# Optimization experiments

Measured on AMD Instinct MI355X. Metric: run time of the kernel, lower is better.

The kernel has to match this reference:

```python
import math
import jax, jax.numpy as jnp
import numpy as np

B, T = 16, 576
HG = WG = 24          # grid_size
DIN = DOUT = 768
NH, HD = 12, 64       # n_heads, head_dim
LD = 256              # latent_dim
SCALES = (1, 2, 4)


def _rel_idx(s):
    """Replicates _build_rel_pos_indices for scale s (static numpy constants)."""
    gh, gw = HG // s, WG // s
    qh, qw = np.meshgrid(np.arange(HG), np.arange(WG), indexing='ij')
    qh, qw = qh.reshape(-1), qw.reshape(-1)                      # (T,)
    kh = np.arange(gh) * s + (s - 1) / 2.0                       # pooled key centers
    kw = np.arange(gw) * s + (s - 1) / 2.0
    kh2, kw2 = np.meshgrid(kh, kw, indexing='ij')
    kh2, kw2 = kh2.reshape(-1), kw2.reshape(-1)                  # (gh*gw,)
    # .astype(int64) truncates toward zero, matching torch .long()
    rel_h = (qh[:, None] - kh2[None, :]).astype(np.int64) + (HG - 1)
    rel_w = (qw[:, None] - kw2[None, :]).astype(np.int64) + (gw - 1)
    return jnp.asarray(rel_h * (2 * gw - 1) + rel_w)             # (T, gh*gw)


def setup_inputs() -> dict:
    key = jax.random.key(0)
    ks = jax.random.split(key, 16)
    std = 0.02
    inp = {
        'x': jax.random.normal(ks[0], (B, T, DIN), dtype=jnp.float32),
        'wq': jax.random.normal(ks[1], (DIN, DOUT), dtype=jnp.float32) * std,
        'wdkv': jax.random.normal(ks[2], (DIN, LD), dtype=jnp.float32) * std,
        'wuk1': jax.random.normal(ks[3], (LD, DOUT), dtype=jnp.float32) * std,
        'wuk2': jax.random.normal(ks[4], (LD, DOUT), dtype=jnp.float32) * std,
        'wuk4': jax.random.normal(ks[5], (LD, DOUT), dtype=jnp.float32) * std,
        'wuv1': jax.random.normal(ks[6], (LD, DOUT), dtype=jnp.float32) * std,
        'wuv2': jax.random.normal(ks[7], (LD, DOUT), dtype=jnp.float32) * std,
        'wuv4': jax.random.normal(ks[8], (LD, DOUT), dtype=jnp.float32) * std,
        'wout': jax.random.normal(ks[12], (DOUT, DOUT), dtype=jnp.float32) * std,
        'bout': jnp.zeros((DOUT,), dtype=jnp.float32),
    }
    # rel-pos bias tables: table_h = 2*HG-1 = 47; table_w = 2*(WG//s)-1
    for j, s in enumerate(SCALES):
        tw = 2 * (WG // s) - 1
        inp[f'tbl{s}'] = jax.random.normal(ks[9 + j], (NH, (2 * HG - 1) * tw),
                                           dtype=jnp.float32) * std
    return inp


def reference(x, wq, wdkv, wuk1, wuk2, wuk4, wuv1, wuv2, wuv4,
              tbl1, tbl2, tbl4, wout, bout):
    b = x.shape[0]
    q = (x @ wq).reshape(b, T, NH, HD).transpose(0, 2, 1, 3)     # (B,H,T,hd)
    lat = x @ wdkv                                                # (B,T,LD)
    lat_sp = lat.reshape(b, HG, WG, LD)
    wuks, wuvs = (wuk1, wuk2, wuk4), (wuv1, wuv2, wuv4)
    tbls = (tbl1, tbl2, tbl4)
    scale = 1.0 / math.sqrt(HD)
    out = jnp.zeros((b, NH, T, HD), x.dtype)
    for i, s in enumerate(SCALES):
        gh, gw = HG // s, WG // s
        if s > 1:  # exact s x s mean pooling (adaptive pool with divisible dims)
            lp = lat_sp.reshape(b, gh, s, gw, s, LD).mean(axis=(2, 4))
        else:
            lp = lat_sp
        lseq = lp.reshape(b, gh * gw, LD)
        k = (lseq @ wuks[i]).reshape(b, gh * gw, NH, HD).transpose(0, 2, 1, 3)
        v = (lseq @ wuvs[i]).reshape(b, gh * gw, NH, HD).transpose(0, 2, 1, 3)
        bias = tbls[i][:, _rel_idx(s)]                            # (H,T,K) gather
        scores = jnp.einsum('bhqd,bhkd->bhqk', q, k) * scale + bias[None]
        w = jax.nn.softmax(scores, axis=-1)
        out = out + jnp.einsum('bhqk,bhkd->bhqd', w, v)
    out = out / len(SCALES)
    ctx = out.transpose(0, 2, 1, 3).reshape(b, T, DOUT)
    return ctx @ wout + bout
```

## Files before the change

kernel.cpp:

```cpp
#include <hip/hip_runtime.h>
#include <hip/hip_bf16.h>
#include <math.h>

#define B_   16
#define T_   576
#define NH_  12

typedef unsigned short u16;
typedef __attribute__((ext_vector_type(8))) short bf16x8;
typedef __attribute__((ext_vector_type(4))) float f32x4;

__device__ __forceinline__ float bf2f(u16 u) {
    union { unsigned int i; float f; } x; x.i = ((unsigned int)u) << 16; return x.f;
}
__device__ __forceinline__ u16 f2bf(float f) {
    union { float f; unsigned int i; } x; x.f = f;
    unsigned int r = x.i + 0x7fffu + ((x.i >> 16) & 1u);
    return (u16)(r >> 16);
}
__device__ __forceinline__ void splitf(float v, u16& h, u16& l) {
    h = f2bf(v);
    l = f2bf(v - bf2f(h));
}
__device__ __forceinline__ void gld_lds16(const u16* g, u16* l) {
    __builtin_amdgcn_global_load_lds(
        (const __attribute__((address_space(1))) unsigned int*)g,
        (__attribute__((address_space(3))) unsigned int*)l, 16, 0, 0);
}
__device__ __forceinline__ float exp2f_(float x) {
#if __has_builtin(__builtin_amdgcn_exp2f)
    return __builtin_amdgcn_exp2f(x);
#else
    return exp2f(x);
#endif
}

__global__ __launch_bounds__(256)
void convert_bf(const float* __restrict__ in, u16* __restrict__ out, int n) {
    const int i8 = (blockIdx.x * 256 + threadIdx.x) * 8;
    if (i8 >= n) return;
    const float4 a = *(const float4*)&in[i8];
    const float4 b = *(const float4*)&in[i8 + 4];
    u16 o[8] = {f2bf(a.x),f2bf(a.y),f2bf(a.z),f2bf(a.w),
                f2bf(b.x),f2bf(b.y),f2bf(b.z),f2bf(b.w)};
    *(bf16x8*)&out[i8] = *(bf16x8*)o;
}

__global__ __launch_bounds__(256)
void prep_weights(const float* __restrict__ wq, const float* __restrict__ wdkv,
                  const float* __restrict__ uk1, const float* __restrict__ uv1,
                  const float* __restrict__ uk2, const float* __restrict__ uv2,
                  const float* __restrict__ uk4, const float* __restrict__ uv4,
                  const float* __restrict__ wout,
                  u16* wqT, u16* wdkvT, u16* uk1T, u16* uv1T, u16* uk2T,
                  u16* uv2T, u16* uk4T, u16* uv4T, u16* woutTh, u16* woutTl) {
    int id = blockIdx.x;
    const float* W; u16* Th; u16* Tl = nullptr; int K, N, gx; bool split = false;
    if (id < 576)       { W = wq;  Th = wqT;  K = 768; N = 768; gx = 24; }
    else if (id < 768)  { id -= 576; W = wdkv; Th = wdkvT; K = 768; N = 256; gx = 8; }
    else if (id < 1920) {
        id -= 768; const int w = id / 192; id -= w * 192;
        const float* Ws[6] = {uk1, uv1, uk2, uv2, uk4, uv4};
        u16* Ts[6] = {uk1T, uv1T, uk2T, uv2T, uk4T, uv4T};
        W = Ws[w]; Th = Ts[w]; K = 256; N = 768; gx = 24;
    } else { id -= 1920; W = wout; Th = woutTh; Tl = woutTl; K = 768; N = 768; gx = 24; split = true; }
    const int bx = id % gx, by = id / gx;
    const int n0 = bx * 32, k0 = by * 32;

    __shared__ float t[32][33];
    const int tid = threadIdx.x;
    const int c  = tid & 31;
    const int r4 = tid >> 5;
#pragma unroll
    for (int i = 0; i < 4; ++i)
        t[r4*4+i][c] = W[(size_t)(k0 + r4*4 + i) * N + n0 + c];
    __syncthreads();
#pragma unroll
    for (int i = 0; i < 4; ++i) {
        const float v = t[c][r4*4+i];
        const size_t o = (size_t)(n0 + r4*4 + i) * K + k0 + c;
        if (split) { u16 h, l; splitf(v, h, l); Th[o] = h; Tl[o] = l; }
        else       { Th[o] = f2bf(v); }
    }
}

template<bool IN_SPLIT, int OM1, int OM2, bool HAS_BIAS>
__global__ __launch_bounds__(256, 2)
void gemm_mfma(const u16* __restrict__ Ah, const u16* __restrict__ Al,
               const u16* __restrict__ B1h, const u16* __restrict__ B1l,
               const u16* __restrict__ B2h,
               const float* __restrict__ bias, float* __restrict__ C1f,
               u16* __restrict__ C1bf, u16* __restrict__ C2bf,
               int M, int N1, int N2, int K, int KSt) {
    __shared__ u16 smem[(IN_SPLIT ? 4 : 2) * 8192];
    const int tid  = threadIdx.x;
    const int wid  = tid >> 6;
    const int lane = tid & 63;
    const int lr   = lane & 15;
    const int kg   = lane >> 4;
    const int wr   = wid >> 1, wc = wid & 1;
    const int m0   = blockIdx.y * 128;
    const int n0   = blockIdx.x * 128;
    const bool second = (OM2 >= 0) && (n0 >= N1);
    const int nb   = second ? n0 - N1 : n0;
    const int subrow = lane >> 3;
    const int gslot  = (lane & 7) ^ subrow;

    const u16* src; int rowbase; bool isA; u16* tile;
    constexpr int NITER = IN_SPLIT ? 16 : 8;
    if (IN_SPLIT) {
        src = (wid == 0) ? Ah : (wid == 1) ? Al : (wid == 2) ? B1h : B1l;
        rowbase = (wid < 2) ? m0 : n0;
        isA = (wid < 2);
        tile = smem + wid * 8192;
    } else {
        const u16* Bsel = second ? B2h : B1h;
        src = (wid < 2) ? Ah : Bsel;
        rowbase = ((wid < 2) ? m0 : nb) + (wid & 1) * 64;
        isA = (wid < 2);
        tile = smem + (wid >> 1) * 8192 + (wid & 1) * 4096;
    }

    f32x4 acc[4][4];
#pragma unroll
    for (int i = 0; i < 4; ++i)
#pragma unroll
        for (int j = 0; j < 4; ++j) acc[i][j] = (f32x4)(0.f);

    for (int k0 = 0; k0 < K; k0 += 64) {
#pragma unroll
        for (int i = 0; i < NITER; ++i) {
            int grow = rowbase + i*8 + subrow;
            if (isA && grow >= M) grow = M - 1;
            gld_lds16(src + (size_t)grow * K + (k0 + gslot * 8), tile + i * 512);
        }
        __syncthreads();
#pragma unroll
        for (int ks = 0; ks < 2; ++ks) {
            const int slot = (ks*4 + kg) ^ (lr & 7);
            bf16x8 ah[4], bh[4], al[4], bl[4];
#pragma unroll
            for (int i = 0; i < 4; ++i) {
                const int offA = (wr*64 + i*16 + lr) * 64 + slot * 8;
                const int offB = (wc*64 + i*16 + lr) * 64 + slot * 8;
                ah[i] = *(const bf16x8*)(smem + offA);
                bh[i] = *(const bf16x8*)(smem + (IN_SPLIT ? 16384 : 8192) + offB);
                if (IN_SPLIT) {
                    al[i] = *(const bf16x8*)(smem + 8192  + offA);
                    bl[i] = *(const bf16x8*)(smem + 24576 + offB);
                }
            }
#pragma unroll
            for (int i = 0; i < 4; ++i)
#pragma unroll
                for (int j = 0; j < 4; ++j) {
                    acc[i][j] = __builtin_amdgcn_mfma_f32_16x16x32_bf16(ah[i], bh[j], acc[i][j], 0, 0, 0);
                    if (IN_SPLIT) {
                        acc[i][j] = __builtin_amdgcn_mfma_f32_16x16x32_bf16(ah[i], bl[j], acc[i][j], 0, 0, 0);
                        acc[i][j] = __builtin_amdgcn_mfma_f32_16x16x32_bf16(al[i], bh[j], acc[i][j], 0, 0, 0);
                    }
                }
        }
        __syncthreads();
    }
    const int rb = lane >> 4;
    float bv[4];
    if (HAS_BIAS) {
#pragma unroll
        for (int j = 0; j < 4; ++j) bv[j] = bias[n0 + wc*64 + j*16 + lr];
    }
#pragma unroll
    for (int i = 0; i < 4; ++i)
#pragma unroll
        for (int e = 0; e < 4; ++e) {
            const int row = m0 + wr*64 + i*16 + rb*4 + e;
            if (row < M) {
#pragma unroll
                for (int j = 0; j < 4; ++j) {
                    const int colw = wc*64 + j*16 + lr;
                    float v = acc[i][j][e];
                    if (HAS_BIAS) v += bv[j];
                    if (!second) {
                        const int col = n0 + colw;
                        if (OM1 == 0) C1f[(size_t)row * N1 + col] = v;
                        else if (OM1 == 1) C1bf[(size_t)row * N1 + col] = f2bf(v);
                        else {
                            const int bidx = row / KSt, key = row - bidx * KSt;
                            C1bf[((size_t)bidx * N1 + col) * KSt + key] = f2bf(v);
                        }
                    } else {
                        const int col = nb + colw;
                        if (OM2 == 1) C2bf[(size_t)row * N2 + col] = f2bf(v);
                        else if (OM2 == 2) {
                            const int bidx = row / KSt, key = row - bidx * KSt;
                            C2bf[((size_t)bidx * N2 + col) * KSt + key] = f2bf(v);
                        }
                    }
                }
            }
        }
}

__global__ __launch_bounds__(256)
void pool_both(const u16* __restrict__ lat, u16* __restrict__ lp2,
               u16* __restrict__ lp4) {
    const int c = threadIdx.x;
    int id = blockIdx.x;
    if (id < 2304) {
        const int b = id / 144, g = id - b*144;
        const int gh = g / 12, gw = g - gh*12;
        const size_t i0 = (((size_t)(b*24 + gh*2))*24 + gw*2)*256 + c;
        const float s = (bf2f(lat[i0]) + bf2f(lat[i0+256]) +
                         bf2f(lat[i0+24*256]) + bf2f(lat[i0+24*256+256])) * 0.25f;
        lp2[(size_t)id*256 + c] = f2bf(s);
    } else {
        id -= 2304;
        const int b = id / 36, g = id - b*36;
        const int gh = g / 6, gw = g - gh*6;
        const size_t base = (((size_t)(b*24 + gh*4))*24 + gw*4)*256 + c;
        float s = 0.f;
#pragma unroll
        for (int i = 0; i < 4; ++i)
#pragma unroll
            for (int j = 0; j < 4; ++j)
                s += bf2f(lat[base + (size_t)(i*24 + j)*256]);
        lp4[(size_t)id*256 + c] = f2bf(s * (1.f/16.f));
    }
}

template<int KS, int GW, int S>
__device__ __forceinline__ void attn_scale(
    const u16* __restrict__ Kbf, const u16* __restrict__ Vt,
    const float* __restrict__ TBL,
    const bf16x8 qa[2], int qh, int qw, int b, int h,
    int tid, int lr, int kg,
    u16 (*Kl)[72], u16 (*Vl)[72], u16* PlW, float* TblL,
    f32x4 octx[4])
{
    constexpr int TW  = 2*GW - 1;
    constexpr int NT  = (KS + 63) / 64;
    constexpr int NTB = 47 * TW;
    constexpr float C1 = 0.18033688011112042f;

    __syncthreads();
    for (int i = tid; i < NTB; i += 256)
        TblL[i] = TBL[(size_t)h * NTB + i] * 1.4426950408889634f;

    const int base1 = (qh + 23)*TW + qw + (GW - 1);
    f32x4 pacc[4];
#pragma unroll
    for (int j = 0; j < 4; ++j) pacc[j] = (f32x4)(0.f);
    float ls = 0.f;

    const int keyS = tid & 63;
    const int c2   = tid >> 6;

    for (int t = 0; t < NT; ++t) {
        const int kt0 = t * 64;
        __syncthreads();
        {
            const u16* kp = Kbf + ((size_t)b*KS + kt0 + keyS)*768 + h*64;
            *(bf16x8*)&Kl[keyS][c2*8]     = *(const bf16x8*)(kp + c2*8);
            *(bf16x8*)&Kl[keyS][(c2+4)*8] = *(const bf16x8*)(kp + (c2+4)*8);
            const u16* vp = Vt + ((size_t)b*768 + h*64 + keyS)*KS;
            const int kb0 = kt0 + c2*8;
            const int kb1 = kt0 + 32 + c2*8;
            if ((KS % 8) == 0 && ((KS % 64) == 0 || kb0 + 8 <= KS)) {
                *(bf16x8*)&Vl[keyS][c2*8] = *(const bf16x8*)(vp + kb0);
            } else {
                bf16x8 vv = {0,0,0,0,0,0,0,0};
#pragma unroll
                for (int u = 0; u < 8; ++u) if (kb0 + u < KS) vv[u] = (short)vp[kb0+u];
                *(bf16x8*)&Vl[keyS][c2*8] = vv;
            }
            if ((KS % 8) == 0 && ((KS % 64) == 0 || kb1 + 8 <= KS)) {
                *(bf16x8*)&Vl[keyS][(c2+4)*8] = *(const bf16x8*)(vp + kb1);
            } else {
                bf16x8 vv = {0,0,0,0,0,0,0,0};
#pragma unroll
                for (int u = 0; u < 8; ++u) if (kb1 + u < KS) vv[u] = (short)vp[kb1+u];
                *(bf16x8*)&Vl[keyS][(c2+4)*8] = vv;
            }
        }
        __syncthreads();

        f32x4 sf[4] = {(f32x4)(0.f), (f32x4)(0.f), (f32x4)(0.f), (f32x4)(0.f)};
        __builtin_amdgcn_s_setprio(1);
#pragma unroll
        for (int ks = 0; ks < 2; ++ks)
#pragma unroll
            for (int g = 0; g < 4; ++g) {
                const bf16x8 kb = *(const bf16x8*)&Kl[g*16 + lr][ks*32 + kg*8];
                sf[g] = __builtin_amdgcn_mfma_f32_16x16x32_bf16(kb, qa[ks], sf[g], 0, 0, 0);
            }
        __builtin_amdgcn_s_setprio(0);

#pragma unroll
        for (int g = 0; g < 4; ++g) {
            const int key0 = kt0 + g*16 + kg*4;
            const bool v4 = ((KS % 64) == 0) || (key0 < KS);
            const int khi  = key0 / GW;
            const int kwi0 = key0 - khi*GW;
            float pv[4];
            if (S == 1) {
                const int idx0 = base1 - khi*TW - kwi0;
#pragma unroll
                for (int e = 0; e < 4; ++e)
                    pv[e] = exp2f_(fmaf(sf[g][e], C1, TblL[idx0 - e]));
            } else if (S == 2) {
                const int dh = qh - 2*khi;
                const int rh = dh - (dh >= 1) + 23;
#pragma unroll
                for (int e = 0; e < 4; ++e) {
                    const int dw = qw - 2*(kwi0 + e);
                    const int rw = dw - (dw >= 1) + (GW - 1);
                    const float x = fmaf(sf[g][e], C1, TblL[rh*TW + rw]);
                    pv[e] = v4 ? exp2f_(x) : 0.f;
                }
            } else {
#pragma unroll
                for (int e = 0; e < 4; ++e) {
                    int kk = kwi0 + e;
                    const int wrap = (kk >= GW);
                    kk -= wrap ? GW : 0;
                    const int kh2 = khi + wrap;
                    const int dh = qh - 4*kh2;
                    const int dw = qw - 4*kk;
                    const int rh = dh - 1 - (dh >= 2) + 23;
                    const int rw = dw - 1 - (dw >= 2) + (GW - 1);
                    const float x = fmaf(sf[g][e], C1, TblL[rh*TW + rw]);
                    pv[e] = v4 ? exp2f_(x) : 0.f;
                }
            }
            ls += (pv[0] + pv[1]) + (pv[2] + pv[3]);
            const unsigned int plo = (unsigned int)f2bf(pv[0]) | ((unsigned int)f2bf(pv[1]) << 16);
            const unsigned int phi = (unsigned int)f2bf(pv[2]) | ((unsigned int)f2bf(pv[3]) << 16);
            *(uint2*)&PlW[lr*72 + g*16 + kg*4] = make_uint2(plo, phi);
        }

        __builtin_amdgcn_s_setprio(1);
#pragma unroll
        for (int ks = 0; ks < 2; ++ks) {
            const bf16x8 pb = *(const bf16x8*)&PlW[lr*72 + ks*32 + kg*8];
#pragma unroll
            for (int j = 0; j < 4; ++j) {
                const bf16x8 vb = *(const bf16x8*)&Vl[j*16 + lr][ks*32 + kg*8];
                pacc[j] = __builtin_amdgcn_mfma_f32_16x16x32_bf16(vb, pb, pacc[j], 0, 0, 0);
            }
        }
        __builtin_amdgcn_s_setprio(0);
    }

    ls += __shfl_xor(ls, 16);
    ls += __shfl_xor(ls, 32);
    const float inv = 1.0f / (3.0f * ls);
#pragma unroll
    for (int j = 0; j < 4; ++j)
#pragma unroll
        for (int e = 0; e < 4; ++e)
            octx[j][e] = fmaf(pacc[j][e], inv, octx[j][e]);
}

__global__ __launch_bounds__(256)
void attn_fused(const u16* __restrict__ Qbf,
                const u16* __restrict__ K1, const u16* __restrict__ V1t,
                const u16* __restrict__ K2, const u16* __restrict__ V2t,
                const u16* __restrict__ K4, const u16* __restrict__ V4t,
                const float* __restrict__ T1, const float* __restrict__ T2,
                const float* __restrict__ T4,
                u16* __restrict__ Ch, u16* __restrict__ Cl) {
    __shared__ u16 Kl[64][72];
    __shared__ u16 Vl[64][72];
    __shared__ u16 Pl[4][16][72];
    __shared__ float TblF[2209];
    const int tid  = threadIdx.x;
    const int wid  = tid >> 6;
    const int lane = tid & 63;
    const int lr   = lane & 15;
    const int kg   = lane >> 4;
    const int bid  = blockIdx.x;
    const int qt   = bid / 192;
    const int bh   = bid - qt*192;
    const int b    = bh / 12;
    const int h    = bh - b*12;
    const int qw0  = qt*64 + wid*16;
    const int q    = qw0 + lr;
    const int qh   = q / 24, qw = q - qh*24;

    bf16x8 qa[2];
    {
        const u16* qp = Qbf + ((size_t)(b*T_) + q)*768 + h*64 + kg*8;
        qa[0] = *(const bf16x8*)qp;
        qa[1] = *(const bf16x8*)(qp + 32);
    }
    f32x4 octx[4];
#pragma unroll
    for (int j = 0; j < 4; ++j) octx[j] = (f32x4)(0.f);
    u16* PlW = &Pl[wid][0][0];

    attn_scale<576,24,1>(K1, V1t, T1, qa, qh, qw, b, h, tid, lr, kg, Kl, Vl, PlW, TblF, octx);
    attn_scale<144,12,2>(K2, V2t, T2, qa, qh, qw, b, h, tid, lr, kg, Kl, Vl, PlW, TblF, octx);
    attn_scale< 36, 6,4>(K4, V4t, T4, qa, qh, qw, b, h, tid, lr, kg, Kl, Vl, PlW, TblF, octx);

    const size_t rowoff = ((size_t)(b*T_) + q)*768 + h*64;
#pragma unroll
    for (int j = 0; j < 4; ++j) {
        ushort4 hv, lv;
        u16 h0,h1,h2,h3, l0,l1,l2,l3;
        splitf(octx[j][0], h0, l0); splitf(octx[j][1], h1, l1);
        splitf(octx[j][2], h2, l2); splitf(octx[j][3], h3, l3);
        hv = make_ushort4(h0,h1,h2,h3); lv = make_ushort4(l0,l1,l2,l3);
        *(ushort4*)&Ch[rowoff + j*16 + kg*4] = hv;
        *(ushort4*)&Cl[rowoff + j*16 + kg*4] = lv;
    }
}

extern "C" void kernel_launch(void* const* d_in, const int* in_sizes, int n_in,
                              void* d_out, int out_size, void* d_ws, size_t ws_size,
                              hipStream_t stream) {
    const float* x    = (const float*)d_in[0];
    const float* wq   = (const float*)d_in[1];
    const float* wdkv = (const float*)d_in[2];
    const float* wuk1 = (const float*)d_in[3];
    const float* wuk2 = (const float*)d_in[4];
    const float* wuk4 = (const float*)d_in[5];
    const float* wuv1 = (const float*)d_in[6];
    const float* wuv2 = (const float*)d_in[7];
    const float* wuv4 = (const float*)d_in[8];
    const float* wout = (const float*)d_in[9];
    const float* bout = (const float*)d_in[10];
    const float* tbl1 = (const float*)d_in[11];
    const float* tbl2 = (const float*)d_in[12];
    const float* tbl4 = (const float*)d_in[13];

    u16* p = (u16*)d_ws;
    u16* x_bf   = p;            p += 7077888;
    u16* q_bf   = p;            p += 7077888;
    u16* lat_bf = p;            p += 2359296;
    u16* lp2_bf = p;            p += 589824;
    u16* lp4_bf = p;            p += 147456;
    u16* wqT    = p;            p += 589824;
    u16* wdkvT  = p;            p += 196608;
    u16* uk1T   = p;            p += 196608;
    u16* uv1T   = p;            p += 196608;
    u16* uk2T   = p;            p += 196608;
    u16* uv2T   = p;            p += 196608;
    u16* uk4T   = p;            p += 196608;
    u16* uv4T   = p;            p += 196608;
    u16* woutTh = p;            p += 589824;
    u16* woutTl = p;            p += 589824;
    u16* k1     = p;            p += 7077888;
    u16* v1t    = p;            p += 7077888;
    u16* k2     = p;            p += 1769472;
    u16* v2t    = p;            p += 1769472;
    u16* k4     = p;            p += 442368;
    u16* v4t    = p;            p += 442368;
    u16* ctxh   = p;            p += 7077888;
    u16* ctxl   = p;            p += 7077888;
    float* outp = (float*)d_out;

    convert_bf<<<3456, 256, 0, stream>>>(x, x_bf, 7077888);
    prep_weights<<<2496, 256, 0, stream>>>(wq, wdkv, wuk1, wuv1, wuk2, wuv2,
                                           wuk4, wuv4, wout,
                                           wqT, wdkvT, uk1T, uv1T, uk2T, uv2T,
                                           uk4T, uv4T, woutTh, woutTl);

    gemm_mfma<false,1,1,false><<<dim3(8,72), 256, 0, stream>>>(
        x_bf, nullptr, wqT, nullptr, wdkvT, nullptr, nullptr, q_bf, lat_bf,
        9216, 768, 256, 768, 0);
    pool_both<<<2880, 256, 0, stream>>>(lat_bf, lp2_bf, lp4_bf);

    gemm_mfma<false,1,2,false><<<dim3(12,72), 256, 0, stream>>>(
        lat_bf, nullptr, uk1T, nullptr, uv1T, nullptr, nullptr, k1, v1t,
        9216, 768, 768, 256, 576);
    gemm_mfma<false,1,2,false><<<dim3(12,18), 256, 0, stream>>>(
        lp2_bf, nullptr, uk2T, nullptr, uv2T, nullptr, nullptr, k2, v2t,
        2304, 768, 768, 256, 144);
    gemm_mfma<false,1,2,false><<<dim3(12,5), 256, 0, stream>>>(
        lp4_bf, nullptr, uk4T, nullptr, uv4T, nullptr, nullptr, k4, v4t,
        576, 768, 768, 256, 36);

    attn_fused<<<9*192, 256, 0, stream>>>(q_bf, k1, v1t, k2, v2t, k4, v4t,
                                          tbl1, tbl2, tbl4, ctxh, ctxl);

    gemm_mfma<true,0,-1,true><<<dim3(6,72), 256, 0, stream>>>(
        ctxh, ctxl, woutTh, woutTl, nullptr, bout, outp, nullptr, nullptr,
        9216, 768, 0, 768, 0);
}
```

Measured before the change: 331.0 us.

## Double-buffer K/V tiles with async LDS loads and merge prep and KV launches

The attention kernel now streams K/V tiles through two LDS buffers with global_load_lds and an XOR swizzle, so the next tile is fetched while the current one is computed. All three scales run as one continuous tile pipeline, and all three bias tables are preloaded once. Separately, the input convert and weight prep are merged into one launch, and the three KV projection GEMMs become a single kernel. The V4 stride is padded to 64 so its tile loads stay in bounds. This cuts launch overhead and global-load stalls, at the cost of more LDS per block (which may lower occupancy) and more complex synchronisation.

After: 293.3 us. 1.13x faster.

```diff
diff --git a/kernel.cpp b/kernel.cpp
--- a/kernel.cpp
+++ b/kernel.cpp
@@ -35,26 +35,32 @@
 #endif
 }
 
+#define VMBAR() do { \
+    asm volatile("s_waitcnt vmcnt(0)" ::: "memory"); \
+    __builtin_amdgcn_s_barrier(); \
+    __builtin_amdgcn_sched_barrier(0); } while (0)
+
 __global__ __launch_bounds__(256)
-void convert_bf(const float* __restrict__ in, u16* __restrict__ out, int n) {
-    const int i8 = (blockIdx.x * 256 + threadIdx.x) * 8;
-    if (i8 >= n) return;
-    const float4 a = *(const float4*)&in[i8];
-    const float4 b = *(const float4*)&in[i8 + 4];
-    u16 o[8] = {f2bf(a.x),f2bf(a.y),f2bf(a.z),f2bf(a.w),
-                f2bf(b.x),f2bf(b.y),f2bf(b.z),f2bf(b.w)};
-    *(bf16x8*)&out[i8] = *(bf16x8*)o;
-}
-
-__global__ __launch_bounds__(256)
-void prep_weights(const float* __restrict__ wq, const float* __restrict__ wdkv,
-                  const float* __restrict__ uk1, const float* __restrict__ uv1,
-                  const float* __restrict__ uk2, const float* __restrict__ uv2,
-                  const float* __restrict__ uk4, const float* __restrict__ uv4,
-                  const float* __restrict__ wout,
-                  u16* wqT, u16* wdkvT, u16* uk1T, u16* uv1T, u16* uk2T,
-                  u16* uv2T, u16* uk4T, u16* uv4T, u16* woutTh, u16* woutTl) {
+void prep_all(const float* __restrict__ x, u16* __restrict__ x_bf,
+              const float* __restrict__ wq, const float* __restrict__ wdkv,
+              const float* __restrict__ uk1, const float* __restrict__ uv1,
+              const float* __restrict__ uk2, const float* __restrict__ uv2,
+              const float* __restrict__ uk4, const float* __restrict__ uv4,
+              const float* __restrict__ wout,
+              u16* wqT, u16* wdkvT, u16* uk1T, u16* uv1T, u16* uk2T,
+              u16* uv2T, u16* uk4T, u16* uv4T, u16* woutTh, u16* woutTl) {
+    __shared__ float t[32][33];
     int id = blockIdx.x;
+    if (id < 3456) {
+        const int i8 = (id * 256 + threadIdx.x) * 8;
+        const float4 a = *(const float4*)&x[i8];
+        const float4 b = *(const float4*)&x[i8 + 4];
+        u16 o[8] = {f2bf(a.x),f2bf(a.y),f2bf(a.z),f2bf(a.w),
+                    f2bf(b.x),f2bf(b.y),f2bf(b.z),f2bf(b.w)};
+        *(bf16x8*)&x_bf[i8] = *(bf16x8*)o;
+        return;
+    }
+    id -= 3456;
     const float* W; u16* Th; u16* Tl = nullptr; int K, N, gx; bool split = false;
     if (id < 576)       { W = wq;  Th = wqT;  K = 768; N = 768; gx = 24; }
     else if (id < 768)  { id -= 576; W = wdkv; Th = wdkvT; K = 768; N = 256; gx = 8; }
@@ -66,8 +72,6 @@
     } else { id -= 1920; W = wout; Th = woutTh; Tl = woutTl; K = 768; N = 768; gx = 24; split = true; }
     const int bx = id % gx, by = id / gx;
     const int n0 = bx * 32, k0 = by * 32;
-
-    __shared__ float t[32][33];
     const int tid = threadIdx.x;
     const int c  = tid & 31;
     const int r4 = tid >> 5;
@@ -85,22 +89,22 @@
 }
 
 template<bool IN_SPLIT, int OM1, int OM2, bool HAS_BIAS>
-__global__ __launch_bounds__(256, 2)
-void gemm_mfma(const u16* __restrict__ Ah, const u16* __restrict__ Al,
+__device__ __forceinline__ void gemm_body(
+               u16* smem, int bx, int by,
+               const u16* __restrict__ Ah, const u16* __restrict__ Al,
                const u16* __restrict__ B1h, const u16* __restrict__ B1l,
                const u16* __restrict__ B2h,
                const float* __restrict__ bias, float* __restrict__ C1f,
                u16* __restrict__ C1bf, u16* __restrict__ C2bf,
-               int M, int N1, int N2, int K, int KSt) {
-    __shared__ u16 smem[(IN_SPLIT ? 4 : 2) * 8192];
+               int M, int N1, int N2, int K, int KStL, int KStS) {
     const int tid  = threadIdx.x;
     const int wid  = tid >> 6;
     const int lane = tid & 63;
     const int lr   = lane & 15;
     const int kg   = lane >> 4;
     const int wr   = wid >> 1, wc = wid & 1;
-    const int m0   = blockIdx.y * 128;
-    const int n0   = blockIdx.x * 128;
+    const int m0   = by * 128;
+    const int n0   = bx * 128;
     const bool second = (OM2 >= 0) && (n0 >= N1);
     const int nb   = second ? n0 - N1 : n0;
     const int subrow = lane >> 3;
@@ -185,20 +189,58 @@
                         if (OM1 == 0) C1f[(size_t)row * N1 + col] = v;
                         else if (OM1 == 1) C1bf[(size_t)row * N1 + col] = f2bf(v);
                         else {
-                            const int bidx = row / KSt, key = row - bidx * KSt;
-                            C1bf[((size_t)bidx * N1 + col) * KSt + key] = f2bf(v);
+                            const int bidx = row / KStL, key = row - bidx * KStL;
+                            C1bf[((size_t)bidx * N1 + col) * KStS + key] = f2bf(v);
                         }
                     } else {
                         const int col = nb + colw;
                         if (OM2 == 1) C2bf[(size_t)row * N2 + col] = f2bf(v);
                         else if (OM2 == 2) {
-                            const int bidx = row / KSt, key = row - bidx * KSt;
-                            C2bf[((size_t)bidx * N2 + col) * KSt + key] = f2bf(v);
+                            const int bidx = row / KStL, key = row - bidx * KStL;
+                            C2bf[((size_t)bidx * N2 + col) * KStS + key] = f2bf(v);
                         }
                     }
                 }
             }
         }
+}
+
+template<bool IN_SPLIT, int OM1, int OM2, bool HAS_BIAS>
+__global__ __launch_bounds__(256, 2)
+void gemm_mfma(const u16* __restrict__ Ah, const u16* __restrict__ Al,
+               const u16* __restrict__ B1h, const u16* __restrict__ B1l,
+               const u16* __restrict__ B2h,
+               const float* __restrict__ bias, float* __restrict__ C1f,
+               u16* __restrict__ C1bf, u16* __restrict__ C2bf,
+               int M, int N1, int N2, int K, int KStL, int KStS) {
+    __shared__ u16 smem[(IN_SPLIT ? 4 : 2) * 8192];
+    gemm_body<IN_SPLIT,OM1,OM2,HAS_BIAS>(smem, blockIdx.x, blockIdx.y,
+        Ah, Al, B1h, B1l, B2h, bias, C1f, C1bf, C2bf, M, N1, N2, K, KStL, KStS);
+}
+
+__global__ __launch_bounds__(256, 2)
+void kv_fused(const u16* __restrict__ lat, const u16* __restrict__ lp2,
+              const u16* __restrict__ lp4,
+              const u16* uk1T, const u16* uv1T, const u16* uk2T,
+              const u16* uv2T, const u16* uk4T, const u16* uv4T,
+              u16* k1, u16* v1t, u16* k2, u16* v2t, u16* k4, u16* v4t) {
+    __shared__ u16 smem[2 * 8192];
+    int bid = blockIdx.x;
+    if (bid < 864) {
+        gemm_body<false,1,2,false>(smem, bid % 12, bid / 12,
+            lat, nullptr, uk1T, nullptr, uv1T, nullptr, nullptr, k1, v1t,
+            9216, 768, 768, 256, 576, 576);
+    } else if (bid < 1080) {
+        bid -= 864;
+        gemm_body<false,1,2,false>(smem, bid % 12, bid / 12,
+            lp2, nullptr, uk2T, nullptr, uv2T, nullptr, nullptr, k2, v2t,
+            2304, 768, 768, 256, 144, 144);
+    } else {
+        bid -= 1080;
+        gemm_body<false,1,2,false>(smem, bid % 12, bid / 12,
+            lp4, nullptr, uk4T, nullptr, uv4T, nullptr, nullptr, k4, v4t,
+            576, 768, 768, 256, 36, 64);
+    }
 }
 
 __global__ __launch_bounds__(256)
@@ -228,80 +270,59 @@
     }
 }
 
+__device__ __forceinline__ void issue_tile(
+    const u16* __restrict__ Kbf, const u16* __restrict__ Vt,
+    int b, int h, int KS, int VSTR, int kt0,
+    u16* Kdst, u16* Vdst, int wid, int lane)
+{
+    const int sub  = lane >> 3;
+    const int srcc = (lane & 7) ^ sub;
+#pragma unroll
+    for (int s = wid; s < 8; s += 4) {
+        const int row = s*8 + sub;
+        int gk = kt0 + row; gk = gk < KS ? gk : KS - 1;
+        gld_lds16(Kbf + ((size_t)b*KS + gk)*768 + h*64 + srcc*8, Kdst + s*512);
+    }
+#pragma unroll
+    for (int s = wid; s < 8; s += 4) {
+        const int row = s*8 + sub;
+        gld_lds16(Vt + ((size_t)(b*768 + h*64 + row))*VSTR + kt0 + srcc*8,
+                  Vdst + s*512);
+    }
+}
+
 template<int KS, int GW, int S>
-__device__ __forceinline__ void attn_scale(
-    const u16* __restrict__ Kbf, const u16* __restrict__ Vt,
-    const float* __restrict__ TBL,
-    const bf16x8 qa[2], int qh, int qw, int b, int h,
-    int tid, int lr, int kg,
-    u16 (*Kl)[72], u16 (*Vl)[72], u16* PlW, float* TblL,
-    f32x4 octx[4])
+__device__ __forceinline__ void attn_tile(
+    int kt0, const u16* __restrict__ Kb, const u16* __restrict__ Vb,
+    const float* __restrict__ TblL, u16* __restrict__ PlW,
+    int qh, int qw, int base1, int lr, int kg,
+    const bf16x8 qa[2], f32x4 pacc[4], float& ls)
 {
-    constexpr int TW  = 2*GW - 1;
-    constexpr int NT  = (KS + 63) / 64;
-    constexpr int NTB = 47 * TW;
+    constexpr int TW = 2*GW - 1;
     constexpr float C1 = 0.18033688011112042f;
 
-    __syncthreads();
-    for (int i = tid; i < NTB; i += 256)
-        TblL[i] = TBL[(size_t)h * NTB + i] * 1.4426950408889634f;
-
-    const int base1 = (qh + 23)*TW + qw + (GW - 1);
-    f32x4 pacc[4];
-#pragma unroll
-    for (int j = 0; j < 4; ++j) pacc[j] = (f32x4)(0.f);
-    float ls = 0.f;
-
-    const int keyS = tid & 63;
-    const int c2   = tid >> 6;
-
-    for (int t = 0; t < NT; ++t) {
-        const int kt0 = t * 64;
-        __syncthreads();
-        {
-            const u16* kp = Kbf + ((size_t)b*KS + kt0 + keyS)*768 + h*64;
-            *(bf16x8*)&Kl[keyS][c2*8]     = *(const bf16x8*)(kp + c2*8);
-            *(bf16x8*)&Kl[keyS][(c2+4)*8] = *(const bf16x8*)(kp + (c2+4)*8);
-            const u16* vp = Vt + ((size_t)b*768 + h*64 + keyS)*KS;
-            const int kb0 = kt0 + c2*8;
-            const int kb1 = kt0 + 32 + c2*8;
-            if ((KS % 8) == 0 && ((KS % 64) == 0 || kb0 + 8 <= KS)) {
-                *(bf16x8*)&Vl[keyS][c2*8] = *(const bf16x8*)(vp + kb0);
-            } else {
-                bf16x8 vv = {0,0,0,0,0,0,0,0};
-#pragma unroll
-                for (int u = 0; u < 8; ++u) if (kb0 + u < KS) vv[u] = (short)vp[kb0+u];
-                *(bf16x8*)&Vl[keyS][c2*8] = vv;
-            }
-            if ((KS % 8) == 0 && ((KS % 64) == 0 || kb1 + 8 <= KS)) {
-                *(bf16x8*)&Vl[keyS][(c2+4)*8] = *(const bf16x8*)(vp + kb1);
-            } else {
-                bf16x8 vv = {0,0,0,0,0,0,0,0};
-#pragma unroll
-                for (int u = 0; u < 8; ++u) if (kb1 + u < KS) vv[u] = (short)vp[kb1+u];
-                *(bf16x8*)&Vl[keyS][(c2+4)*8] = vv;
-            }
+    f32x4 sf[4];
+#pragma unroll
+    for (int g = 0; g < 4; ++g) sf[g] = (f32x4)(0.f);
+    __builtin_amdgcn_s_setprio(1);
+#pragma unroll
+    for (int ks = 0; ks < 2; ++ks)
+#pragma unroll
+        for (int g = 0; g < 4; ++g) {
+            const int rc = (ks*4 + kg) ^ (lr & 7);
+            const bf16x8 kb = *(const bf16x8*)(Kb + (g*16 + lr)*64 + rc*8);
+            sf[g] = __builtin_amdgcn_mfma_f32_16x16x32_bf16(kb, qa[ks], sf[g], 0, 0, 0);
         }
-        __syncthreads();
-
-        f32x4 sf[4] = {(f32x4)(0.f), (f32x4)(0.f), (f32x4)(0.f), (f32x4)(0.f)};
-        __builtin_amdgcn_s_setprio(1);
-#pragma unroll
-        for (int ks = 0; ks < 2; ++ks)
-#pragma unroll
-            for (int g = 0; g < 4; ++g) {
-                const bf16x8 kb = *(const bf16x8*)&Kl[g*16 + lr][ks*32 + kg*8];
-                sf[g] = __builtin_amdgcn_mfma_f32_16x16x32_bf16(kb, qa[ks], sf[g], 0, 0, 0);
-            }
-        __builtin_amdgcn_s_setprio(0);
-
-#pragma unroll
-        for (int g = 0; g < 4; ++g) {
-            const int key0 = kt0 + g*16 + kg*4;
-            const bool v4 = ((KS % 64) == 0) || (key0 < KS);
+    __builtin_amdgcn_s_setprio(0);
+
+#pragma unroll
+    for (int g = 0; g < 4; ++g) {
+        const int key0 = kt0 + g*16 + kg*4;
+        const bool v4 = ((KS % 64) == 0) || (key0 < KS);
+        float pv[4];
+        if (v4) {
             const int khi  = key0 / GW;
             const int kwi0 = key0 - khi*GW;
-            float pv[4];
             if (S == 1) {
                 const int idx0 = base1 - khi*TW - kwi0;
 #pragma unroll
@@ -314,8 +335,7 @@
                 for (int e = 0; e < 4; ++e) {
                     const int dw = qw - 2*(kwi0 + e);
                     const int rw = dw - (dw >= 1) + (GW - 1);
-                    const float x = fmaf(sf[g][e], C1, TblL[rh*TW + rw]);
-                    pv[e] = v4 ? exp2f_(x) : 0.f;
+                    pv[e] = exp2f_(fmaf(sf[g][e], C1, TblL[rh*TW + rw]));
                 }
             } else {
 #pragma unroll
@@ -328,37 +348,45 @@
                     const int dw = qw - 4*kk;
                     const int rh = dh - 1 - (dh >= 2) + 23;
                     const int rw = dw - 1 - (dw >= 2) + (GW - 1);
-                    const float x = fmaf(sf[g][e], C1, TblL[rh*TW + rw]);
-                    pv[e] = v4 ? exp2f_(x) : 0.f;
+                    pv[e] = exp2f_(fmaf(sf[g][e], C1, TblL[rh*TW + rw]));
                 }
             }
-            ls += (pv[0] + pv[1]) + (pv[2] + pv[3]);
-            const unsigned int plo = (unsigned int)f2bf(pv[0]) | ((unsigned int)f2bf(pv[1]) << 16);
-            const unsigned int phi = (unsigned int)f2bf(pv[2]) | ((unsigned int)f2bf(pv[3]) << 16);
-            *(uint2*)&PlW[lr*72 + g*16 + kg*4] = make_uint2(plo, phi);
+        } else {
+            pv[0] = pv[1] = pv[2] = pv[3] = 0.f;
         }
-
-        __builtin_amdgcn_s_setprio(1);
-#pragma unroll
-        for (int ks = 0; ks < 2; ++ks) {
-            const bf16x8 pb = *(const bf16x8*)&PlW[lr*72 + ks*32 + kg*8];
-#pragma unroll
-            for (int j = 0; j < 4; ++j) {
-                const bf16x8 vb = *(const bf16x8*)&Vl[j*16 + lr][ks*32 + kg*8];
-                pacc[j] = __builtin_amdgcn_mfma_f32_16x16x32_bf16(vb, pb, pacc[j], 0, 0, 0);
-            }
+        ls += (pv[0] + pv[1]) + (pv[2] + pv[3]);
+        const unsigned int plo = (unsigned int)f2bf(pv[0]) | ((unsigned int)f2bf(pv[1]) << 16);
+        const unsigned int phi = (unsigned int)f2bf(pv[2]) | ((unsigned int)f2bf(pv[3]) << 16);
+        *(uint2*)&PlW[lr*72 + g*16 + kg*4] = make_uint2(plo, phi);
+    }
+
+    __builtin_amdgcn_s_setprio(1);
+#pragma unroll
+    for (int ks = 0; ks < 2; ++ks) {
+        const bf16x8 pb = *(const bf16x8*)(PlW + lr*72 + ks*32 + kg*8);
+#pragma unroll
+        for (int j = 0; j < 4; ++j) {
+            const int rc = (ks*4 + kg) ^ (lr & 7);
+            const bf16x8 vb = *(const bf16x8*)(Vb + (j*16 + lr)*64 + rc*8);
+            pacc[j] = __builtin_amdgcn_mfma_f32_16x16x32_bf16(vb, pb, pacc[j], 0, 0, 0);
         }
-        __builtin_amdgcn_s_setprio(0);
-    }
-
-    ls += __shfl_xor(ls, 16);
-    ls += __shfl_xor(ls, 32);
-    const float inv = 1.0f / (3.0f * ls);
-#pragma unroll
-    for (int j = 0; j < 4; ++j)
+    }
+    __builtin_amdgcn_s_setprio(0);
+}
+
+__device__ __forceinline__ void fold3(f32x4 pacc[4], float& ls, f32x4 octx[4]) {
+    float l = ls;
+    l += __shfl_xor(l, 16);
+    l += __shfl_xor(l, 32);
+    const float inv = 1.0f / (3.0f * l);
+#pragma unroll
+    for (int j = 0; j < 4; ++j) {
 #pragma unroll
         for (int e = 0; e < 4; ++e)
             octx[j][e] = fmaf(pacc[j][e], inv, octx[j][e]);
+        pacc[j] = (f32x4)(0.f);
+    }
+    ls = 0.f;
 }
 
 __global__ __launch_bounds__(256)
@@ -369,10 +397,9 @@
                 const float* __restrict__ T1, const float* __restrict__ T2,
                 const float* __restrict__ T4,
                 u16* __restrict__ Ch, u16* __restrict__ Cl) {
-    __shared__ u16 Kl[64][72];
-    __shared__ u16 Vl[64][72];
-    __shared__ u16 Pl[4][16][72];
-    __shared__ float TblF[2209];
+    __shared__ u16 KlA[4096], KlB[4096], VlA[4096], VlB[4096];
+    __shared__ u16 Pl[4][16*72];
+    __shared__ float Tb[3807];
     const int tid  = threadIdx.x;
     const int wid  = tid >> 6;
     const int lane = tid & 63;
@@ -386,6 +413,16 @@
     const int qw0  = qt*64 + wid*16;
     const int q    = qw0 + lr;
     const int qh   = q / 24, qw = q - qh*24;
+    const int base1 = (qh + 23)*47 + qw + 23;
+    constexpr float LOG2E = 1.4426950408889634f;
+
+    issue_tile(K1, V1t, b, h, 576, 576, 0, KlA, VlA, wid, lane);
+    for (int i = tid; i < 2209; i += 256) Tb[i]        = T1[(size_t)h*2209 + i] * LOG2E;
+    for (int i = tid; i < 1081; i += 256) Tb[2209 + i] = T2[(size_t)h*1081 + i] * LOG2E;
+    for (int i = tid; i < 517;  i += 256) Tb[3290 + i] = T4[(size_t)h*517  + i] * LOG2E;
+    asm volatile("s_waitcnt vmcnt(0) lgkmcnt(0)" ::: "memory");
+    __builtin_amdgcn_s_barrier();
+    __builtin_amdgcn_sched_barrier(0);
 
     bf16x8 qa[2];
     {
@@ -393,25 +430,47 @@
         qa[0] = *(const bf16x8*)qp;
         qa[1] = *(const bf16x8*)(qp + 32);
     }
-    f32x4 octx[4];
-#pragma unroll
-    for (int j = 0; j < 4; ++j) octx[j] = (f32x4)(0.f);
-    u16* PlW = &Pl[wid][0][0];
-
-    attn_scale<576,24,1>(K1, V1t, T1, qa, qh, qw, b, h, tid, lr, kg, Kl, Vl, PlW, TblF, octx);
-    attn_scale<144,12,2>(K2, V2t, T2, qa, qh, qw, b, h, tid, lr, kg, Kl, Vl, PlW, TblF, octx);
-    attn_scale< 36, 6,4>(K4, V4t, T4, qa, qh, qw, b, h, tid, lr, kg, Kl, Vl, PlW, TblF, octx);
+    f32x4 octx[4], pacc[4];
+#pragma unroll
+    for (int j = 0; j < 4; ++j) { octx[j] = (f32x4)(0.f); pacc[j] = (f32x4)(0.f); }
+    float ls = 0.f;
+    u16* PlW = &Pl[wid][0];
+
+#pragma unroll 2
+    for (int t = 0; t < 8; ++t) {
+        issue_tile(K1, V1t, b, h, 576, 576, (t+1)*64,
+                   (t&1) ? KlA : KlB, (t&1) ? VlA : VlB, wid, lane);
+        attn_tile<576,24,1>(t*64, (t&1) ? KlB : KlA, (t&1) ? VlB : VlA,
+                            Tb, PlW, qh, qw, base1, lr, kg, qa, pacc, ls);
+        VMBAR();
+    }
+    issue_tile(K2, V2t, b, h, 144, 144, 0, KlB, VlB, wid, lane);
+    attn_tile<576,24,1>(512, KlA, VlA, Tb, PlW, qh, qw, base1, lr, kg, qa, pacc, ls);
+    VMBAR();
+    fold3(pacc, ls, octx);
+
+    issue_tile(K2, V2t, b, h, 144, 144, 64, KlA, VlA, wid, lane);
+    attn_tile<144,12,2>(0, KlB, VlB, Tb + 2209, PlW, qh, qw, 0, lr, kg, qa, pacc, ls);
+    VMBAR();
+    issue_tile(K2, V2t, b, h, 144, 144, 128, KlB, VlB, wid, lane);
+    attn_tile<144,12,2>(64, KlA, VlA, Tb + 2209, PlW, qh, qw, 0, lr, kg, qa, pacc, ls);
+    VMBAR();
+    issue_tile(K4, V4t, b, h, 36, 64, 0, KlA, VlA, wid, lane);
+    attn_tile<144,12,2>(128, KlB, VlB, Tb + 2209, PlW, qh, qw, 0, lr, kg, qa, pacc, ls);
+    VMBAR();
+    fold3(pacc, ls, octx);
+
+    attn_tile<36,6,4>(0, KlA, VlA, Tb + 3290, PlW, qh, qw, 0, lr, kg, qa, pacc, ls);
+    fold3(pacc, ls, octx);
 
     const size_t rowoff = ((size_t)(b*T_) + q)*768 + h*64;
 #pragma unroll
     for (int j = 0; j < 4; ++j) {
-        ushort4 hv, lv;
         u16 h0,h1,h2,h3, l0,l1,l2,l3;
         splitf(octx[j][0], h0, l0); splitf(octx[j][1], h1, l1);
         splitf(octx[j][2], h2, l2); splitf(octx[j][3], h3, l3);
-        hv = make_ushort4(h0,h1,h2,h3); lv = make_ushort4(l0,l1,l2,l3);
-        *(ushort4*)&Ch[rowoff + j*16 + kg*4] = hv;
-        *(ushort4*)&Cl[rowoff + j*16 + kg*4] = lv;
+        *(ushort4*)&Ch[rowoff + j*16 + kg*4] = make_ushort4(h0,h1,h2,h3);
+        *(ushort4*)&Cl[rowoff + j*16 + kg*4] = make_ushort4(l0,l1,l2,l3);
     }
 }
 
@@ -454,36 +513,29 @@
     u16* k2     = p;            p += 1769472;
     u16* v2t    = p;            p += 1769472;
     u16* k4     = p;            p += 442368;
-    u16* v4t    = p;            p += 442368;
+    u16* v4t    = p;            p += 786432;
     u16* ctxh   = p;            p += 7077888;
     u16* ctxl   = p;            p += 7077888;
     float* outp = (float*)d_out;
 
-    convert_bf<<<3456, 256, 0, stream>>>(x, x_bf, 7077888);
-    prep_weights<<<2496, 256, 0, stream>>>(wq, wdkv, wuk1, wuv1, wuk2, wuv2,
-                                           wuk4, wuv4, wout,
-                                           wqT, wdkvT, uk1T, uv1T, uk2T, uv2T,
-                                           uk4T, uv4T, woutTh, woutTl);
+    prep_all<<<5952, 256, 0, stream>>>(x, x_bf, wq, wdkv, wuk1, wuv1, wuk2,
+                                       wuv2, wuk4, wuv4, wout,
+                                       wqT, wdkvT, uk1T, uv1T, uk2T, uv2T,
+                                       uk4T, uv4T, woutTh, woutTl);
 
     gemm_mfma<false,1,1,false><<<dim3(8,72), 256, 0, stream>>>(
         x_bf, nullptr, wqT, nullptr, wdkvT, nullptr, nullptr, q_bf, lat_bf,
-        9216, 768, 256, 768, 0);
+        9216, 768, 256, 768, 0, 0);
     pool_both<<<2880, 256, 0, stream>>>(lat_bf, lp2_bf, lp4_bf);
 
-    gemm_mfma<false,1,2,false><<<dim3(12,72), 256, 0, stream>>>(
-        lat_bf, nullptr, uk1T, nullptr, uv1T, nullptr, nullptr, k1, v1t,
-        9216, 768, 768, 256, 576);
-    gemm_mfma<false,1,2,false><<<dim3(12,18), 256, 0, stream>>>(
-        lp2_bf, nullptr, uk2T, nullptr, uv2T, nullptr, nullptr, k2, v2t,
-        2304, 768, 768, 256, 144);
-    gemm_mfma<false,1,2,false><<<dim3(12,5), 256, 0, stream>>>(
-        lp4_bf, nullptr, uk4T, nullptr, uv4T, nullptr, nullptr, k4, v4t,
-        576, 768, 768, 256, 36);
+    kv_fused<<<1140, 256, 0, stream>>>(lat_bf, lp2_bf, lp4_bf,
+                                       uk1T, uv1T, uk2T, uv2T, uk4T, uv4T,
+                                       k1, v1t, k2, v2t, k4, v4t);
 
     attn_fused<<<9*192, 256, 0, stream>>>(q_bf, k1, v1t, k2, v2t, k4, v4t,
                                           tbl1, tbl2, tbl4, ctxh, ctxl);
 
     gemm_mfma<true,0,-1,true><<<dim3(6,72), 256, 0, stream>>>(
         ctxh, ctxl, woutTh, woutTl, nullptr, bout, outp, nullptr, nullptr,
-        9216, 768, 0, 768, 0);
-}
+        9216, 768, 0, 768, 0, 0);
+}
```
